# Performance work log

Measured on AMD Instinct MI355X. Metric: run time of the kernel, lower is better.

Reference implementation:

```python
import jax, jax.numpy as jnp
import numpy as np

B, N, NPOINT, K = 8, 8192, 1024, 32
MLP = [64, 64, 128]
EPS = 1e-5  # torch BatchNorm2d default eps


def setup_inputs() -> dict:
    key = jax.random.key(0)
    ks = jax.random.split(key, 1 + 2 * len(MLP))
    inp = {"xyz": jax.random.normal(ks[0], (B, N, 3), jnp.float32)}
    last = 3
    for i, o in enumerate(MLP):
        inp[f"w{i}"] = jax.random.normal(ks[1 + 2 * i], (o, last), jnp.float32) / np.float32(np.sqrt(last))
        inp[f"b{i}"] = jax.random.normal(ks[2 + 2 * i], (o,), jnp.float32) * 0.01
        inp[f"g{i}"] = jnp.ones((o,), jnp.float32)   # BN weight
        inp[f"be{i}"] = jnp.zeros((o,), jnp.float32)  # BN bias
        last = o
    return inp


def farthest_point_sample(xyz, npoint):
    # Sequential FPS; deterministic start at index 0 (original torch uses randint).
    Bb, Nn, _ = xyz.shape

    def step(carry, _):
        distance, farthest = carry
        centroid = jnp.take_along_axis(xyz, farthest[:, None, None], axis=1)  # [B,1,3]
        dist = jnp.sum((xyz - centroid) ** 2, -1)                              # [B,N]
        distance = jnp.minimum(distance, dist)
        nxt = jnp.argmax(distance, -1)
        return (distance, nxt), farthest

    init = (jnp.full((Bb, Nn), 1e10, xyz.dtype), jnp.zeros((Bb,), jnp.int32))
    _, cents = jax.lax.scan(step, init, None, length=npoint)
    return cents.T  # [B, npoint]


def _forward(xyz, params):
    fps_idx = farthest_point_sample(xyz, NPOINT)
    fps_idx = jax.lax.stop_gradient(fps_idx)
    new_xyz = jnp.take_along_axis(xyz, fps_idx[:, :, None], axis=1)  # [B,npoint,3]
    # squared pairwise distances [B, npoint, N]
    d = (jnp.sum(new_xyz ** 2, -1)[:, :, None]
         + jnp.sum(xyz ** 2, -1)[:, None, :]
         - 2.0 * jnp.einsum('bmc,bnc->bmn', new_xyz, xyz))
    _, idx = jax.lax.top_k(-d, K)  # k nearest neighbors, [B,npoint,k]
    grouped = jax.vmap(lambda pts, i: pts[i])(xyz, idx)  # [B,npoint,k,3]
    feat = grouped - new_xyz[:, :, None, :]              # grouped_xyz_norm
    # 1x1 Conv2d + BatchNorm2d(training stats) + ReLU stack
    for (w, b, g, be) in params:
        feat = jnp.einsum('bnkc,oc->bnko', feat, w) + b
        mu = jnp.mean(feat, axis=(0, 1, 2))
        var = jnp.var(feat, axis=(0, 1, 2))
        feat = g * (feat - mu) * jax.lax.rsqrt(var + EPS) + be
        feat = jax.nn.relu(feat)
    out = jnp.max(feat, axis=2)             # max over k neighbors -> [B,npoint,Cout]
    return new_xyz, jnp.transpose(out, (0, 2, 1))  # [B,npoint,3], [B,Cout,npoint]


def reference(xyz, w0, b0, g0, be0, w1, b1, g1, be1, w2, b2, g2, be2):
    params = [(w0, b0, g0, be0), (w1, b1, g1, be1), (w2, b2, g2, be2)]
    return _forward(xyz, params)
```

## Files before the change

kernel.cpp:

```cpp
#include <hip/hip_runtime.h>

#define NN_ 8192
#define MM_ 1024
#define NROWS_ 262144

#define DPP_UMAX64(K, CTRL)                                                     \
  {                                                                             \
    const int lo_ = (int)(unsigned int)(K);                                     \
    const int hi_ = (int)(unsigned int)((K) >> 32);                             \
    const int slo_ = __builtin_amdgcn_update_dpp(lo_, lo_, (CTRL), 0xf, 0xf, false); \
    const int shi_ = __builtin_amdgcn_update_dpp(hi_, hi_, (CTRL), 0xf, 0xf, false); \
    const unsigned long long ok_ =                                              \
        ((unsigned long long)(unsigned int)shi_ << 32) | (unsigned int)slo_;    \
    (K) = (ok_ > (K)) ? ok_ : (K);                                              \
  }
#define DPP_UMIN64(K, CTRL)                                                     \
  {                                                                             \
    const int lo_ = (int)(unsigned int)(K);                                     \
    const int hi_ = (int)(unsigned int)((K) >> 32);                             \
    const int slo_ = __builtin_amdgcn_update_dpp(lo_, lo_, (CTRL), 0xf, 0xf, false); \
    const int shi_ = __builtin_amdgcn_update_dpp(hi_, hi_, (CTRL), 0xf, 0xf, false); \
    const unsigned long long ok_ =                                              \
        ((unsigned long long)(unsigned int)shi_ << 32) | (unsigned int)slo_;    \
    (K) = (ok_ < (K)) ? ok_ : (K);                                              \
  }

#define WAVE_STATS(T, ACC, PO_S, PO_Q)                                          \
  {                                                                             \
    _Pragma("unroll") for (int o_ = 0; o_ < 64; ++o_)                           \
        (T)[o_ * 64 + ((lane + o_) & 63)] = (ACC)[o_];                          \
    float s_ = 0.0f, q_ = 0.0f;                                                 \
    _Pragma("unroll") for (int j_ = 0; j_ < 64; ++j_) {                         \
      const float v_ = (T)[lane * 64 + ((j_ + lane) & 63)];                     \
      s_ += v_;                                                                 \
      q_ = fmaf(v_, v_, q_);                                                    \
    }                                                                           \
    (PO_S)[lane] = s_;                                                          \
    (PO_Q)[lane] = q_;                                                          \
  }

__global__ __launch_bounds__(256, 1) void fps_kernel(const float* __restrict__ xyz,
                                                     float* __restrict__ dout) {
  const int b = blockIdx.x;
  const int tid = threadIdx.x;
  const float* xb = xyz + (size_t)b * NN_ * 3;

  __shared__ float s_x[NN_], s_y[NN_], s_z[NN_];
  __shared__ float s_out[3 * MM_];
  __shared__ __align__(16) unsigned long long s_key[2][4];

  for (int i = tid; i < NN_; i += 256) {
    s_x[i] = xb[3 * i + 0];
    s_y[i] = xb[3 * i + 1];
    s_z[i] = xb[3 * i + 2];
  }
  __syncthreads();

  const int base = 32 * tid;
  float4 rx[8], ry[8], rz[8];
#pragma unroll
  for (int q = 0; q < 8; ++q) {
    rx[q] = *(const float4*)&s_x[base + 4 * q];
    ry[q] = *(const float4*)&s_y[base + 4 * q];
    rz[q] = *(const float4*)&s_z[base + 4 * q];
  }
  asm volatile("" ::: "memory");

  float pd[32];
#pragma unroll
  for (int j = 0; j < 32; ++j) pd[j] = 1e10f;

  const int lane = tid & 63;
  const int wv = tid >> 6;

  float cx = s_x[0], cy = s_y[0], cz = s_z[0];

  for (int it = 0; it < MM_; ++it) {
    if (tid == 0) {
      s_out[it * 3 + 0] = cx;
      s_out[it * 3 + 1] = cy;
      s_out[it * 3 + 2] = cz;
    }
    if (it == MM_ - 1) break;

    float ld = -1.0f;
    int lj = 0;
#define FPS_UPD(PX, PY, PZ, J)                                                 \
    {                                                                          \
      const float dx = __fsub_rn(PX, cx);                                      \
      const float dy = __fsub_rn(PY, cy);                                      \
      const float dz = __fsub_rn(PZ, cz);                                      \
      const float dist = __fadd_rn(                                            \
          __fadd_rn(__fmul_rn(dx, dx), __fmul_rn(dy, dy)), __fmul_rn(dz, dz)); \
      const float nd = fminf(pd[J], dist);                                     \
      pd[J] = nd;                                                              \
      if (nd > ld) { ld = nd; lj = (J); }                                      \
    }
#pragma unroll
    for (int q = 0; q < 8; ++q) {
      FPS_UPD(rx[q].x, ry[q].x, rz[q].x, 4 * q + 0)
      FPS_UPD(rx[q].y, ry[q].y, rz[q].y, 4 * q + 1)
      FPS_UPD(rx[q].z, ry[q].z, rz[q].z, 4 * q + 2)
      FPS_UPD(rx[q].w, ry[q].w, rz[q].w, 4 * q + 3)
    }
#undef FPS_UPD

    unsigned long long key =
        ((unsigned long long)__float_as_uint(ld) << 32) |
        (unsigned int)(8191 - (base + lj));
    DPP_UMAX64(key, 0x111)
    DPP_UMAX64(key, 0x112)
    DPP_UMAX64(key, 0x114)
    DPP_UMAX64(key, 0x118)
    DPP_UMAX64(key, 0x142)
    DPP_UMAX64(key, 0x143)
    if (lane == 63) s_key[it & 1][wv] = key;
    __syncthreads();

    const ulonglong2 ka = *(const ulonglong2*)&s_key[it & 1][0];
    const ulonglong2 kb = *(const ulonglong2*)&s_key[it & 1][2];
    unsigned long long best = (ka.x > ka.y) ? ka.x : ka.y;
    const unsigned long long bb = (kb.x > kb.y) ? kb.x : kb.y;
    best = (best > bb) ? best : bb;
    const int win = 8191 - (int)(unsigned int)(best & 0xFFFFFFFFu);
    cx = s_x[win];
    cy = s_y[win];
    cz = s_z[win];
  }

  __syncthreads();
  float* outx = dout + (size_t)b * MM_ * 3;
#pragma unroll
  for (int i = 0; i < 12; ++i) outx[i * 256 + tid] = s_out[i * 256 + tid];
}

__global__ __launch_bounds__(64) void knn_kernel(const float* __restrict__ xyz,
                                                 const float* __restrict__ dout,
                                                 int* __restrict__ knn) {
  __shared__ float dl[128][64];
  const int lane = threadIdx.x;
  const int center = blockIdx.x;
  const int b = center >> 10;
  const int m = center & 1023;
  const float* xb = xyz + (size_t)b * NN_ * 3;
  const float* cp = dout + (size_t)b * MM_ * 3 + m * 3;
  const float cx = cp[0], cy = cp[1], cz = cp[2];
  const float sm = __fadd_rn(__fadd_rn(__fmul_rn(cx, cx), __fmul_rn(cy, cy)),
                             __fmul_rn(cz, cz));

  float gd[16];
  int gj[16];
#pragma unroll
  for (int g = 0; g < 16; ++g) {
#pragma unroll
    for (int t = 0; t < 8; ++t) {
      const int jj = g * 8 + t;
      const int p = jj * 64 + lane;
      const float x = xb[p * 3 + 0];
      const float y = xb[p * 3 + 1];
      const float z = xb[p * 3 + 2];
      const float sn = __fadd_rn(__fadd_rn(__fmul_rn(x, x), __fmul_rn(y, y)),
                                 __fmul_rn(z, z));
      const float dt = __fmaf_rn(cz, z, __fmaf_rn(cy, y, __fmul_rn(cx, x)));
      const float d = __fsub_rn(__fadd_rn(sm, sn), __fmul_rn(2.0f, dt));
      dl[jj][lane] = d;
      if (t == 0) { gd[g] = d; gj[g] = jj; }
      else if (d < gd[g]) { gd[g] = d; gj[g] = jj; }
    }
  }

  float ldv = gd[0];
  int ljj = gj[0];
#pragma unroll
  for (int g = 1; g < 16; ++g) {
    if (gd[g] < ldv) { ldv = gd[g]; ljj = gj[g]; }
  }
  unsigned db = __float_as_uint(ldv);
  unsigned mono = (db & 0x80000000u) ? ~db : (db | 0x80000000u);
  unsigned long long mykey =
      ((unsigned long long)mono << 32) | (unsigned int)(ljj * 64 + lane);

  int out_p = 0;
  const float INF = __int_as_float(0x7f800000);
  for (int r = 0; r < 32; ++r) {
    unsigned long long kk = mykey;
    DPP_UMIN64(kk, 0x111)
    DPP_UMIN64(kk, 0x112)
    DPP_UMIN64(kk, 0x114)
    DPP_UMIN64(kk, 0x118)
    DPP_UMIN64(kk, 0x142)
    DPP_UMIN64(kk, 0x143)
    const int lp = __builtin_amdgcn_readlane((int)(unsigned int)(kk & 0xFFFFFFFFull), 63);
    if (lane == r) out_p = lp;
    const int wl = lp & 63;
    if (lane == wl) {
      const int jjs = lp >> 6;
      const int gs = jjs >> 3;
      dl[jjs][lane] = INF;
      float md = INF;
      int mj = 0;
#pragma unroll
      for (int t = 0; t < 8; ++t) {
        const int jj2 = gs * 8 + t;
        const float v = dl[jj2][lane];
        if (v < md) { md = v; mj = jj2; }
      }
#pragma unroll
      for (int g = 0; g < 16; ++g) {
        if (g == gs) { gd[g] = md; gj[g] = mj; }
      }
      float nldv = gd[0];
      int nljj = gj[0];
#pragma unroll
      for (int g = 1; g < 16; ++g) {
        if (gd[g] < nldv) { nldv = gd[g]; nljj = gj[g]; }
      }
      const unsigned ndb = __float_as_uint(nldv);
      const unsigned nmono = (ndb & 0x80000000u) ? ~ndb : (ndb | 0x80000000u);
      mykey = ((unsigned long long)nmono << 32) |
              (unsigned int)(nljj * 64 + lane);
    }
  }
  if (lane < 32) knn[center * 32 + lane] = out_p;
}

__global__ void prep_kernel(const float* __restrict__ w1, const float* __restrict__ w2,
                            float* __restrict__ w1t, float* __restrict__ w2t) {
  const int t = blockIdx.x * 256 + threadIdx.x;
  if (t < 4096) { const int o = t >> 6, c = t & 63; w1t[c * 64 + o] = w1[t]; }
  if (t < 8192) { const int o = t >> 6, c = t & 63; w2t[c * 128 + o] = w2[t]; }
}

__global__ __launch_bounds__(256) void s1_kernel(const float* __restrict__ xyz,
                                                 const float* __restrict__ dout,
                                                 const int* __restrict__ knn,
                                                 const float* __restrict__ w0,
                                                 const float* __restrict__ b0,
                                                 float* __restrict__ part1) {
  __shared__ float tw[4 * 4096];
  const int tid = threadIdx.x;
  const int r = blockIdx.x * 256 + tid;
  const int cid = r >> 5;
  const int b = cid >> 10;
  const int m = cid & 1023;
  const int idx = knn[r];
  const float* pp = xyz + ((size_t)b * NN_ + idx) * 3;
  const float* cc = dout + ((size_t)b * MM_ + m) * 3;
  const float fx = pp[0] - cc[0];
  const float fy = pp[1] - cc[1];
  const float fz = pp[2] - cc[2];
  float acc[64];
#pragma unroll
  for (int o = 0; o < 64; ++o)
    acc[o] = fmaf(w0[o * 3 + 2], fz, fmaf(w0[o * 3 + 1], fy, fmaf(w0[o * 3 + 0], fx, b0[o])));
  const int lane = tid & 63;
  const int wv = tid >> 6;
  float* T = &tw[wv * 4096];
  float* po = part1 + ((size_t)blockIdx.x * 4 + wv) * 128;
  WAVE_STATS(T, acc, po, po + 64)
}

__global__ __launch_bounds__(256) void rstat_kernel(const float* __restrict__ part, int C,
                                                    const float* __restrict__ g,
                                                    const float* __restrict__ be,
                                                    float* __restrict__ sc,
                                                    float* __restrict__ sh) {
  const int c = blockIdx.x;
  const int tid = threadIdx.x;
  float S = 0.0f, Q = 0.0f;
  for (int i = tid; i < 4096; i += 256) {
    S += part[(size_t)i * 2 * C + c];
    Q += part[(size_t)i * 2 * C + C + c];
  }
  const int lane = tid & 63;
#pragma unroll
  for (int mk = 1; mk < 64; mk <<= 1) { S += __shfl_xor(S, mk, 64); Q += __shfl_xor(Q, mk, 64); }
  __shared__ float rs[4], rq[4];
  if (lane == 0) { rs[tid >> 6] = S; rq[tid >> 6] = Q; }
  __syncthreads();
  if (tid == 0) {
    S = rs[0] + rs[1] + rs[2] + rs[3];
    Q = rq[0] + rq[1] + rq[2] + rq[3];
    const float mean = S * (1.0f / 262144.0f);
    const float var = fmaf(-mean, mean, Q * (1.0f / 262144.0f));
    const float s = g[c] * rsqrtf(var + 1e-5f);
    sc[c] = s;
    sh[c] = fmaf(-mean, s, be[c]);
  }
}

template <int STAGE>
__global__ __launch_bounds__(256) void chain_kernel(
    const float* __restrict__ xyz, const float* __restrict__ dout,
    const int* __restrict__ knn,
    const float* __restrict__ w0, const float* __restrict__ b0,
    const float* __restrict__ w1t, const float* __restrict__ b1,
    const float* __restrict__ w2t, const float* __restrict__ b2,
    const float* __restrict__ sc1, const float* __restrict__ sh1,
    const float* __restrict__ sc2, const float* __restrict__ sh2,
    const float* __restrict__ sc3, const float* __restrict__ sh3,
    float* __restrict__ part, float* __restrict__ outp,
    float* __restrict__ a2g, int cached) {
  __shared__ float f[64 * 256];
  const int tid = threadIdx.x;
  const int r = blockIdx.x * 256 + tid;
  const int cid = r >> 5;
  const int b = cid >> 10;
  const int m = cid & 1023;
  const int lane = tid & 63;
  const int wv = tid >> 6;

  float a2[64];
  if (STAGE == 2 || !cached) {
    const int idx = knn[r];
    const float* pp = xyz + ((size_t)b * NN_ + idx) * 3;
    const float* cc = dout + ((size_t)b * MM_ + m) * 3;
    const float fx = pp[0] - cc[0];
    const float fy = pp[1] - cc[1];
    const float fz = pp[2] - cc[2];
    float acc[64];
#pragma unroll
    for (int o = 0; o < 64; ++o)
      acc[o] = fmaf(w0[o * 3 + 2], fz, fmaf(w0[o * 3 + 1], fy, fmaf(w0[o * 3 + 0], fx, b0[o])));
#pragma unroll
    for (int o = 0; o < 64; ++o)
      f[o * 256 + tid] = fmaxf(fmaf(acc[o], sc1[o], sh1[o]), 0.0f);
#pragma unroll
    for (int o = 0; o < 64; ++o) a2[o] = b1[o];
#pragma unroll 4
    for (int c = 0; c < 64; ++c) {
      const float x = f[c * 256 + tid];
#pragma unroll
      for (int o = 0; o < 64; ++o) a2[o] = fmaf(w1t[c * 64 + o], x, a2[o]);
    }
  } else {
#pragma unroll
    for (int o = 0; o < 64; ++o) a2[o] = a2g[(size_t)o * NROWS_ + r];
  }

  if constexpr (STAGE == 2) {
    if (cached) {
#pragma unroll
      for (int o = 0; o < 64; ++o) a2g[(size_t)o * NROWS_ + r] = a2[o];
    }
    __syncthreads();
    float* T = &f[wv * 4096];
    float* po = part + ((size_t)blockIdx.x * 4 + wv) * 128;
    WAVE_STATS(T, a2, po, po + 64)
    return;
  }
#pragma unroll
  for (int o = 0; o < 64; ++o)
    f[o * 256 + tid] = fmaxf(fmaf(a2[o], sc2[o], sh2[o]), 0.0f);
  if constexpr (STAGE == 3) {
    float a3l[64], a3h[64];
#pragma unroll
    for (int o = 0; o < 64; ++o) { a3l[o] = b2[o]; a3h[o] = b2[64 + o]; }
#pragma unroll 2
    for (int c = 0; c < 64; ++c) {
      const float x = f[c * 256 + tid];
#pragma unroll
      for (int o = 0; o < 64; ++o) a3l[o] = fmaf(w2t[c * 128 + o], x, a3l[o]);
#pragma unroll
      for (int o = 0; o < 64; ++o) a3h[o] = fmaf(w2t[c * 128 + 64 + o], x, a3h[o]);
    }
    __syncthreads();
    float* T = &f[wv * 4096];
    float* po = part + ((size_t)blockIdx.x * 4 + wv) * 256;
    WAVE_STATS(T, a3l, po, po + 128)
    WAVE_STATS(T, a3h, po + 64, po + 192)
    return;
  }
#pragma unroll
  for (int h = 0; h < 2; ++h) {
    float a3[64];
#pragma unroll
    for (int o = 0; o < 64; ++o) a3[o] = b2[h * 64 + o];
#pragma unroll 4
    for (int c = 0; c < 64; ++c) {
      const float x = f[c * 256 + tid];
#pragma unroll
      for (int o = 0; o < 64; ++o) a3[o] = fmaf(w2t[c * 128 + h * 64 + o], x, a3[o]);
    }
#pragma unroll
    for (int o = 0; o < 64; ++o) {
      float v = fmaxf(fmaf(a3[o], sc3[h * 64 + o], sh3[h * 64 + o]), 0.0f);
#pragma unroll
      for (int mk = 1; mk < 32; mk <<= 1) v = fmaxf(v, __shfl_xor(v, mk, 64));
      if ((lane & 31) == 0)
        outp[24576 + (size_t)b * 131072 + (size_t)(h * 64 + o) * 1024 + m] = v;
    }
  }
}

extern "C" void kernel_launch(void* const* d_in, const int* in_sizes, int n_in,
                              void* d_out, int out_size, void* d_ws, size_t ws_size,
                              hipStream_t stream) {
  const float* xyz = (const float*)d_in[0];
  const float* w0 = (const float*)d_in[1];
  const float* b0 = (const float*)d_in[2];
  const float* g0 = (const float*)d_in[3];
  const float* be0 = (const float*)d_in[4];
  const float* w1 = (const float*)d_in[5];
  const float* b1 = (const float*)d_in[6];
  const float* g1 = (const float*)d_in[7];
  const float* be1 = (const float*)d_in[8];
  const float* w2 = (const float*)d_in[9];
  const float* b2 = (const float*)d_in[10];
  const float* g2 = (const float*)d_in[11];
  const float* be2 = (const float*)d_in[12];
  float* out = (float*)d_out;
  char* ws = (char*)d_ws;

  int* knn = (int*)ws;
  float* part1 = (float*)(ws + (size_t)1 * (1 << 20));
  float* part2 = (float*)(ws + (size_t)3 * (1 << 20));
  float* part3 = (float*)(ws + (size_t)5 * (1 << 20));
  float* sc1 = (float*)(ws + (size_t)9 * (1 << 20));
  float* sh1 = sc1 + 64;
  float* sc2 = sh1 + 64;
  float* sh2 = sc2 + 64;
  float* sc3 = sh2 + 64;
  float* sh3 = sc3 + 128;
  float* w1t = sh3 + 128;
  float* w2t = w1t + 4096;
  float* a2g = (float*)(ws + ((size_t)16 << 20));
  const int cached = (ws_size >= ((size_t)81 << 20)) ? 1 : 0;

  fps_kernel<<<8, 256, 0, stream>>>(xyz, out);
  knn_kernel<<<8192, 64, 0, stream>>>(xyz, out, knn);
  prep_kernel<<<32, 256, 0, stream>>>(w1, w2, w1t, w2t);
  s1_kernel<<<1024, 256, 0, stream>>>(xyz, out, knn, w0, b0, part1);
  rstat_kernel<<<64, 256, 0, stream>>>(part1, 64, g0, be0, sc1, sh1);
  chain_kernel<2><<<1024, 256, 0, stream>>>(xyz, out, knn, w0, b0, w1t, b1, w2t, b2,
                                            sc1, sh1, sc2, sh2, sc3, sh3, part2, out,
                                            a2g, cached);
  rstat_kernel<<<64, 256, 0, stream>>>(part2, 64, g1, be1, sc2, sh2);
  chain_kernel<3><<<1024, 256, 0, stream>>>(xyz, out, knn, w0, b0, w1t, b1, w2t, b2,
                                            sc1, sh1, sc2, sh2, sc3, sh3, part3, out,
                                            a2g, cached);
  rstat_kernel<<<128, 256, 0, stream>>>(part3, 128, g2, be2, sc3, sh3);
  chain_kernel<4><<<1024, 256, 0, stream>>>(xyz, out, knn, w0, b0, w1t, b1, w2t, b2,
                                            sc1, sh1, sc2, sh2, sc3, sh3, part3, out,
                                            a2g, cached);
}
```

Before: 1.481 ms.

## Fuse BN stat reductions into producer kernels via last-block atomic counter

Removes the three separate rstat_kernel launches and instead has the last block to finish each producer kernel (found through an atomic counter and threadfence) reduce the partial sums and write the BN scale/shift. The weight transpose from prep_kernel is folded into fps_kernel. This cuts launch count and inter-kernel gaps, but the final reduction now runs on a single 256-thread block in the tail, and a memset is added to reset the counters.

```diff
diff --git a/kernel.cpp b/kernel.cpp
--- a/kernel.cpp
+++ b/kernel.cpp
@@ -39,11 +39,64 @@
     (PO_Q)[lane] = q_;                                                          \
   }
 
+__device__ __forceinline__ void lastblock_rstat(const float* part, int C, int rows,
+                                                const float* g, const float* be,
+                                                float* sc, float* sh,
+                                                unsigned* cnt, int nblocks, int tid) {
+  __threadfence();
+  __syncthreads();
+  __shared__ int amLast;
+  if (tid == 0) {
+    const unsigned t = atomicAdd(cnt, 1u);
+    amLast = (t == (unsigned)(nblocks - 1));
+  }
+  __syncthreads();
+  if (!amLast) return;
+  __threadfence();
+  const int c = tid % C;
+  const int strip = tid / C;
+  const int nstrips = 256 / C;
+  const int per = rows / nstrips;
+  float S = 0.0f, Q = 0.0f;
+  for (int i = strip * per; i < (strip + 1) * per; ++i) {
+    S += part[(size_t)i * 2 * C + c];
+    Q += part[(size_t)i * 2 * C + C + c];
+  }
+  __shared__ float rs[256], rq[256];
+  rs[tid] = S;
+  rq[tid] = Q;
+  __syncthreads();
+  if (tid < C) {
+    float Ss = rs[tid], Qs = rq[tid];
+    for (int s2 = 1; s2 < nstrips; ++s2) { Ss += rs[s2 * C + tid]; Qs += rq[s2 * C + tid]; }
+    const float mean = Ss * (1.0f / 262144.0f);
+    const float var = fmaf(-mean, mean, Qs * (1.0f / 262144.0f));
+    const float s = g[tid] * rsqrtf(var + 1e-5f);
+    sc[tid] = s;
+    sh[tid] = fmaf(-mean, s, be[tid]);
+  }
+}
+
 __global__ __launch_bounds__(256, 1) void fps_kernel(const float* __restrict__ xyz,
-                                                     float* __restrict__ dout) {
+                                                     float* __restrict__ dout,
+                                                     const float* __restrict__ w1,
+                                                     const float* __restrict__ w2,
+                                                     float* __restrict__ w1t,
+                                                     float* __restrict__ w2t) {
   const int b = blockIdx.x;
   const int tid = threadIdx.x;
   const float* xb = xyz + (size_t)b * NN_ * 3;
+
+  for (int i = b * 256 + tid; i < 12288; i += 2048) {
+    if (i < 4096) {
+      const int o = i >> 6, c = i & 63;
+      w1t[c * 64 + o] = w1[i];
+    } else {
+      const int j = i - 4096;
+      const int o = j >> 6, c = j & 63;
+      w2t[c * 128 + o] = w2[j];
+    }
+  }
 
   __shared__ float s_x[NN_], s_y[NN_], s_z[NN_];
   __shared__ float s_out[3 * MM_];
@@ -224,19 +277,17 @@
   if (lane < 32) knn[center * 32 + lane] = out_p;
 }
 
-__global__ void prep_kernel(const float* __restrict__ w1, const float* __restrict__ w2,
-                            float* __restrict__ w1t, float* __restrict__ w2t) {
-  const int t = blockIdx.x * 256 + threadIdx.x;
-  if (t < 4096) { const int o = t >> 6, c = t & 63; w1t[c * 64 + o] = w1[t]; }
-  if (t < 8192) { const int o = t >> 6, c = t & 63; w2t[c * 128 + o] = w2[t]; }
-}
-
 __global__ __launch_bounds__(256) void s1_kernel(const float* __restrict__ xyz,
                                                  const float* __restrict__ dout,
                                                  const int* __restrict__ knn,
                                                  const float* __restrict__ w0,
                                                  const float* __restrict__ b0,
-                                                 float* __restrict__ part1) {
+                                                 float* __restrict__ part1,
+                                                 const float* __restrict__ g0,
+                                                 const float* __restrict__ be0,
+                                                 float* __restrict__ sc1,
+                                                 float* __restrict__ sh1,
+                                                 unsigned* __restrict__ cnt) {
   __shared__ float tw[4 * 4096];
   const int tid = threadIdx.x;
   const int r = blockIdx.x * 256 + tid;
@@ -258,35 +309,7 @@
   float* T = &tw[wv * 4096];
   float* po = part1 + ((size_t)blockIdx.x * 4 + wv) * 128;
   WAVE_STATS(T, acc, po, po + 64)
-}
-
-__global__ __launch_bounds__(256) void rstat_kernel(const float* __restrict__ part, int C,
-                                                    const float* __restrict__ g,
-                                                    const float* __restrict__ be,
-                                                    float* __restrict__ sc,
-                                                    float* __restrict__ sh) {
-  const int c = blockIdx.x;
-  const int tid = threadIdx.x;
-  float S = 0.0f, Q = 0.0f;
-  for (int i = tid; i < 4096; i += 256) {
-    S += part[(size_t)i * 2 * C + c];
-    Q += part[(size_t)i * 2 * C + C + c];
-  }
-  const int lane = tid & 63;
-#pragma unroll
-  for (int mk = 1; mk < 64; mk <<= 1) { S += __shfl_xor(S, mk, 64); Q += __shfl_xor(Q, mk, 64); }
-  __shared__ float rs[4], rq[4];
-  if (lane == 0) { rs[tid >> 6] = S; rq[tid >> 6] = Q; }
-  __syncthreads();
-  if (tid == 0) {
-    S = rs[0] + rs[1] + rs[2] + rs[3];
-    Q = rq[0] + rq[1] + rq[2] + rq[3];
-    const float mean = S * (1.0f / 262144.0f);
-    const float var = fmaf(-mean, mean, Q * (1.0f / 262144.0f));
-    const float s = g[c] * rsqrtf(var + 1e-5f);
-    sc[c] = s;
-    sh[c] = fmaf(-mean, s, be[c]);
-  }
+  lastblock_rstat(part1, 64, 4096, g0, be0, sc1, sh1, cnt, 1024, tid);
 }
 
 template <int STAGE>
@@ -300,7 +323,10 @@
     const float* __restrict__ sc2, const float* __restrict__ sh2,
     const float* __restrict__ sc3, const float* __restrict__ sh3,
     float* __restrict__ part, float* __restrict__ outp,
-    float* __restrict__ a2g, int cached) {
+    float* __restrict__ a2g, int cached,
+    const float* __restrict__ gN, const float* __restrict__ beN,
+    float* __restrict__ scw, float* __restrict__ shw,
+    unsigned* __restrict__ cnt) {
   __shared__ float f[64 * 256];
   const int tid = threadIdx.x;
   const int r = blockIdx.x * 256 + tid;
@@ -347,6 +373,7 @@
     float* T = &f[wv * 4096];
     float* po = part + ((size_t)blockIdx.x * 4 + wv) * 128;
     WAVE_STATS(T, a2, po, po + 64)
+    lastblock_rstat(part, 64, 4096, gN, beN, scw, shw, cnt, 1024, tid);
     return;
   }
 #pragma unroll
@@ -369,6 +396,7 @@
     float* po = part + ((size_t)blockIdx.x * 4 + wv) * 256;
     WAVE_STATS(T, a3l, po, po + 128)
     WAVE_STATS(T, a3h, po + 64, po + 192)
+    lastblock_rstat(part, 128, 4096, gN, beN, scw, shw, cnt, 1024, tid);
     return;
   }
 #pragma unroll
@@ -424,23 +452,24 @@
   float* sh3 = sc3 + 128;
   float* w1t = sh3 + 128;
   float* w2t = w1t + 4096;
+  unsigned* cnt = (unsigned*)(w2t + 8192);
   float* a2g = (float*)(ws + ((size_t)16 << 20));
   const int cached = (ws_size >= ((size_t)81 << 20)) ? 1 : 0;
 
-  fps_kernel<<<8, 256, 0, stream>>>(xyz, out);
+  hipMemsetAsync(cnt, 0, 3 * sizeof(unsigned), stream);
+  fps_kernel<<<8, 256, 0, stream>>>(xyz, out, w1, w2, w1t, w2t);
   knn_kernel<<<8192, 64, 0, stream>>>(xyz, out, knn);
-  prep_kernel<<<32, 256, 0, stream>>>(w1, w2, w1t, w2t);
-  s1_kernel<<<1024, 256, 0, stream>>>(xyz, out, knn, w0, b0, part1);
-  rstat_kernel<<<64, 256, 0, stream>>>(part1, 64, g0, be0, sc1, sh1);
+  s1_kernel<<<1024, 256, 0, stream>>>(xyz, out, knn, w0, b0, part1,
+                                      g0, be0, sc1, sh1, cnt + 0);
   chain_kernel<2><<<1024, 256, 0, stream>>>(xyz, out, knn, w0, b0, w1t, b1, w2t, b2,
                                             sc1, sh1, sc2, sh2, sc3, sh3, part2, out,
-                                            a2g, cached);
-  rstat_kernel<<<64, 256, 0, stream>>>(part2, 64, g1, be1, sc2, sh2);
+                                            a2g, cached, g1, be1, sc2, sh2, cnt + 1);
   chain_kernel<3><<<1024, 256, 0, stream>>>(xyz, out, knn, w0, b0, w1t, b1, w2t, b2,
                                             sc1, sh1, sc2, sh2, sc3, sh3, part3, out,
-                                            a2g, cached);
-  rstat_kernel<<<128, 256, 0, stream>>>(part3, 128, g2, be2, sc3, sh3);
+                                            a2g, cached, g2, be2, sc3, sh3, cnt + 2);
   chain_kernel<4><<<1024, 256, 0, stream>>>(xyz, out, knn, w0, b0, w1t, b1, w2t, b2,
                                             sc1, sh1, sc2, sh2, sc3, sh3, part3, out,
-                                            a2g, cached);
-}
+                                            a2g, cached, (const float*)nullptr,
+                                            (const float*)nullptr, (float*)nullptr,
+                                            (float*)nullptr, (unsigned*)nullptr);
+}
```

Result: slower. 2.332 ms (+57.4%).
